# Kernel tuning notes

Hardware: AMD Instinct MI355X
Metric: run time of the kernel (lower is better)

## Reference

```python
import jax, jax.numpy as jnp
import numpy as np

B = 2048

def _conv(x, w, b, stride):
    y = jax.lax.conv_general_dilated(x, w, (stride, stride), 'VALID',
                                     dimension_numbers=('NCHW', 'OIHW', 'NCHW'))
    return y + b[None, :, None, None]

def _local_conv(x, w, b):
    # w: (Ho, Wo, Co, Ci, kh, kw), b: (Ho, Wo, Co); stride 1, valid
    Ho, Wo, Co, Ci, kh, kw = w.shape
    # patches: (B, Ci, kh*kw, Ho, Wo) -- sliding windows, small fixed loop over kernel taps
    patches = jnp.stack([x[:, :, i:i + Ho, j:j + Wo]
                         for i in range(kh) for j in range(kw)], axis=2)
    wf = w.reshape(Ho, Wo, Co, Ci, kh * kw)
    y = jnp.einsum('bcphw,hwocp->bohw', patches, wf)
    return y + jnp.transpose(b, (2, 0, 1))[None]

def setup_inputs() -> dict:
    key = jax.random.key(0)
    ks = jax.random.split(key, 18)
    s = 0.05
    inp = {
        'x': jax.random.normal(ks[0], (B, 5, 60, 60), dtype=jnp.float32),
        'info': jax.random.normal(ks[1], (B, 8), dtype=jnp.float32),
        'w1': jax.random.normal(ks[2], (32, 5, 3, 3), dtype=jnp.float32) * s,
        'b1': jnp.zeros((32,), dtype=jnp.float32),
        'w2a': jax.random.normal(ks[3], (64, 32, 3, 3), dtype=jnp.float32) * s,
        'b2a': jnp.zeros((64,), dtype=jnp.float32),
        'w2b': jax.random.normal(ks[4], (64, 64, 3, 3), dtype=jnp.float32) * s,
        'b2b': jnp.zeros((64,), dtype=jnp.float32),
        'lw3': jax.random.normal(ks[5], (9, 9, 64, 64, 5, 5), dtype=jnp.float32) * s,
        'lb3': jnp.zeros((9, 9, 64), dtype=jnp.float32),
        'lw4': jax.random.normal(ks[6], (5, 5, 64, 64, 5, 5), dtype=jnp.float32) * s,
        'lb4': jnp.zeros((5, 5, 64), dtype=jnp.float32),
        'lw5': jax.random.normal(ks[7], (3, 3, 64, 64, 3, 3), dtype=jnp.float32) * s,
        'lb5': jnp.zeros((3, 3, 64), dtype=jnp.float32),
        'hw': jax.random.normal(ks[8], (2, 584), dtype=jnp.float32) * s,
        'hb': jnp.zeros((2,), dtype=jnp.float32),
    }
    return inp

def reference(x, info, w1, b1, w2a, b2a, w2b, b2b, lw3, lb3, lw4, lb4, lw5, lb5, hw, hb):
    h = jnp.tanh(_conv(x, w1, b1, 2))            # (B,32,29,29)
    h = jnp.tanh(_conv(h, w2a, b2a, 1))          # (B,64,27,27)
    h = jnp.tanh(_conv(h, w2b, b2b, 2))          # (B,64,13,13)
    h = jnp.tanh(_local_conv(h, lw3, lb3))       # (B,64,9,9)
    h = jnp.tanh(_local_conv(h, lw4, lb4))       # (B,64,5,5)
    h = jnp.tanh(_local_conv(h, lw5, lb5))       # (B,64,3,3)
    h = h.reshape(h.shape[0], -1)                # (B,576)
    h = jnp.concatenate([h, info], axis=1)       # (B,584)
    logits = h @ hw.T + hb                       # (B,2)
    return jax.nn.softmax(logits, axis=1)
```

## Files before the change

kernel.cpp:

```cpp
#include <hip/hip_runtime.h>
#include <stdint.h>

#define THREADS 256

typedef short bf16x8 __attribute__((ext_vector_type(8)));
typedef float f32x4 __attribute__((ext_vector_type(4)));
typedef unsigned uint2_ __attribute__((ext_vector_type(2)));
typedef unsigned short ushort4_ __attribute__((ext_vector_type(4)));

#define GPTR(x) ((const __attribute__((address_space(1))) void*)(x))
#define LPTR(x) ((__attribute__((address_space(3))) void*)(x))

__device__ __forceinline__ unsigned short f2bf(float v) {
  unsigned u = __builtin_bit_cast(unsigned, v);
  u = (u + 0x7fff + ((u >> 16) & 1)) >> 16;
  return (unsigned short)u;
}
__device__ __forceinline__ float bf2f(unsigned short h) {
  return __builtin_bit_cast(float, (unsigned)h << 16);
}
__device__ __forceinline__ float fast_tanh(float x) {
  return 1.f - 2.f / (__expf(2.f * x) + 1.f);
}

__global__ void pack_w1t(const float* __restrict__ w1, float* __restrict__ w1t) {
  int idx = blockIdx.x * THREADS + threadIdx.x;
  if (idx >= 45 * 32) return;
  int t = idx >> 5, co = idx & 31;
  w1t[t * 32 + co] = w1[co * 45 + t];
}

__global__ void __launch_bounds__(256) conv1_direct(
    const float* __restrict__ x, const float* __restrict__ w1t,
    const float* __restrict__ bias, unsigned short* __restrict__ out, int Bc,
    int bstart) {
  constexpr int CI = 5, CO = 32, IH = 60, IW = 60, OH = 29, OW = 29;
  constexpr int RB = 8, NRB = 4;

  __shared__ unsigned short xs[CI * 17 * 60];

  const int tid = threadIdx.x;
  const int b = blockIdx.x / NRB;
  const int qb = blockIdx.x % NRB;
  const int oh0 = qb * RB;
  const int rows = min(RB, OH - oh0);
  const int ih0 = oh0 * 2;
  const int ihn = rows * 2 + 1;

  const float* xp = x + (size_t)(bstart + b) * (CI * IH * IW);

  const int nf4 = CI * ihn * 15;
  for (int i = tid; i < nf4; i += 256) {
    int col = i % 15;
    int row = i / 15;
    int ci = row / ihn, r = row % ihn;
    float4 v = ((const float4*)xp)[(ci * IH + ih0 + r) * 15 + col];
    ushort4_ o;
    o[0] = f2bf(v.x);
    o[1] = f2bf(v.y);
    o[2] = f2bf(v.z);
    o[3] = f2bf(v.w);
    ((ushort4_*)xs)[row * 15 + col] = o;
  }
  __syncthreads();

  if (tid >= rows * OW) return;
  const int r = tid / OW, c = tid % OW;
  const int base = (r * 2) * 60 + c * 2;
  const int cstr = ihn * 60;

  float acc[32];
#pragma unroll
  for (int co = 0; co < 32; co++) acc[co] = bias[co];

#pragma unroll
  for (int ci = 0; ci < CI; ci++)
#pragma unroll
    for (int kh = 0; kh < 3; kh++)
#pragma unroll
      for (int kw = 0; kw < 3; kw++) {
        const float v = bf2f(xs[ci * cstr + base + kh * 60 + kw]);
        const float* wt = w1t + ((ci * 3 + kh) * 3 + kw) * 32;
#pragma unroll
        for (int co = 0; co < 32; co++) acc[co] = fmaf(v, wt[co], acc[co]);
      }

  const int p = (oh0 + r) * OW + c;
  unsigned short* op = out + ((size_t)p * Bc + b) * CO;
#pragma unroll
  for (int cq = 0; cq < 4; cq++) {
    bf16x8 o;
#pragma unroll
    for (int j = 0; j < 8; j++) o[j] = (short)f2bf(fast_tanh(acc[cq * 8 + j]));
    *(bf16x8*)(op + cq * 8) = o;
  }
}

template <int CI, int KS>
__global__ void __launch_bounds__(THREADS) pack_w(const float* __restrict__ w,
                                                  unsigned short* __restrict__ wp,
                                                  int npos) {
  constexpr int K = CI * KS * KS;
  constexpr int S = K / 32;
  int idx = blockIdx.x * THREADS + threadIdx.x;
  int total = npos * S * 2048;
  if (idx >= total) return;
  int e = idx & 7;
  int lane = (idx >> 3) & 63;
  int mt = (idx >> 9) & 3;
  int rest = idx >> 11;
  int s = rest % S, pos = rest / S;
  int co = mt * 16 + (lane & 15);
  int k = s * 32 + (lane >> 4) * 8 + e;
  int tap = k / CI, ci = k % CI;
  int kh = tap / KS, kw = tap % KS;
  float v = w[((((size_t)pos * 64 + co) * CI + ci) * KS + kh) * KS + kw];
  wp[idx] = f2bf(v);
}

template <int CI, int IH, int IW, int OH, int OW, int KS, int ST, bool LOCAL, int BT>
__global__ void __launch_bounds__(256) conv_mfma(
    const unsigned short* __restrict__ X, const unsigned short* __restrict__ Wp,
    const float* __restrict__ bias, unsigned short* __restrict__ Y, int Bc) {
  constexpr int S = CI * KS * KS / 32;
  constexpr int NPOS = OH * OW;
  constexpr int BW = BT / 64;
  constexpr int CW = 4 / BW;
  constexpr int MT = 4 / CW;

  __shared__ unsigned short aT[2][2048];

  const int tid = threadIdx.x;
  const int lane = tid & 63;
  const int wu = tid >> 6;
  const int n = lane & 15, g = lane >> 4;
  const int bw = wu % BW, cw = wu / BW;

  int wg = blockIdx.x;
  {
    const int nwg = gridDim.x;
    const int q = nwg >> 3, rr = nwg & 7;
    const int xcd = wg & 7, l = wg >> 3;
    wg = (xcd < rr ? xcd * (q + 1) : rr * (q + 1) + (xcd - rr) * q) + l;
  }
  const int pos = wg % NPOS;
  const int btile = wg / NPOS;
  const int oh = pos / OW, ow = pos % OW;
  const int b0 = btile * BT + bw * 64;

  const unsigned short* Wpp = Wp + (LOCAL ? (size_t)pos * (S * 2048) : 0);

  f32x4 acc[MT][4] = {};

  const int bA = b0 + n;

  __builtin_amdgcn_global_load_lds(GPTR(Wpp + tid * 8), LPTR(&aT[0][tid * 8]), 16, 0, 0);

  int buf = 0;
  for (int s = 0; s < S; s++) {
    __syncthreads();
    if (s + 1 < S)
      __builtin_amdgcn_global_load_lds(GPTR(Wpp + (s + 1) * 2048 + tid * 8),
                                       LPTR(&aT[buf ^ 1][tid * 8]), 16, 0, 0);

    const int tap = (s * 32) / CI;
    const int ci0 = (s * 32) % CI + g * 8;
    const int kh = tap / KS, kw = tap % KS;
    const int pin = (oh * ST + kh) * IW + (ow * ST + kw);
    const unsigned short* xb = X + ((size_t)pin * Bc + bA) * CI + ci0;

    bf16x8 bfr[4];
#pragma unroll
    for (int j = 0; j < 4; j++) bfr[j] = *(const bf16x8*)(xb + j * 16 * CI);

    bf16x8 af[MT];
#pragma unroll
    for (int mt = 0; mt < MT; mt++)
      af[mt] = *(const bf16x8*)(&aT[buf][((cw * MT + mt) * 64 + lane) * 8]);

#pragma unroll
    for (int mt = 0; mt < MT; mt++)
#pragma unroll
      for (int j = 0; j < 4; j++)
        acc[mt][j] =
            __builtin_amdgcn_mfma_f32_16x16x32_bf16(af[mt], bfr[j], acc[mt][j], 0, 0, 0);
    buf ^= 1;
  }

#pragma unroll
  for (int mt = 0; mt < MT; mt++) {
#pragma unroll
    for (int j = 0; j < 4; j++) {
      unsigned short o[4];
#pragma unroll
      for (int r = 0; r < 4; r++) {
        const int co = (cw * MT + mt) * 16 + g * 4 + r;
        const float bv = LOCAL ? bias[pos * 64 + co] : bias[co];
        o[r] = f2bf(fast_tanh(acc[mt][j][r] + bv));
      }
      const int b = b0 + j * 16 + n;
      uint2_ pk;
      pk[0] = (unsigned)o[0] | ((unsigned)o[1] << 16);
      pk[1] = (unsigned)o[2] | ((unsigned)o[3] << 16);
      *(uint2_*)(Y + ((size_t)pos * Bc + b) * 64 + (cw * MT + mt) * 16 + g * 4) = pk;
    }
  }
}

__global__ void head_k(const unsigned short* __restrict__ h5,
                       const float* __restrict__ info, const float* __restrict__ hw,
                       const float* __restrict__ hb, float* __restrict__ out, int Bc,
                       int bstart) {
  int b = blockIdx.x * THREADS + threadIdx.x;
  if (b >= Bc) return;
  float l0 = hb[0], l1 = hb[1];
  for (int pos = 0; pos < 9; pos++) {
#pragma unroll
    for (int cb = 0; cb < 8; cb++) {
      bf16x8 v8 = *(const bf16x8*)(h5 + ((size_t)pos * Bc + b) * 64 + cb * 8);
#pragma unroll
      for (int j = 0; j < 8; j++) {
        float v = bf2f((unsigned short)v8[j]);
        int f = (cb * 8 + j) * 9 + pos;
        l0 = fmaf(v, hw[f], l0);
        l1 = fmaf(v, hw[584 + f], l1);
      }
    }
  }
#pragma unroll
  for (int k = 0; k < 8; k++) {
    float v = info[(size_t)(bstart + b) * 8 + k];
    l0 = fmaf(v, hw[576 + k], l0);
    l1 = fmaf(v, hw[584 + 576 + k], l1);
  }
  float m = fmaxf(l0, l1);
  float e0 = __expf(l0 - m), e1 = __expf(l1 - m);
  float s = e0 + e1;
  out[(size_t)(bstart + b) * 2 + 0] = e0 / s;
  out[(size_t)(bstart + b) * 2 + 1] = e1 / s;
}


extern "C" void kernel_launch(void* const* d_in, const int* in_sizes, int n_in,
                              void* d_out, int out_size, void* d_ws, size_t ws_size,
                              hipStream_t stream) {
  const float* x = (const float*)d_in[0];
  const float* info = (const float*)d_in[1];
  const float* w1 = (const float*)d_in[2];
  const float* b1 = (const float*)d_in[3];
  const float* w2a = (const float*)d_in[4];
  const float* b2a = (const float*)d_in[5];
  const float* w2b = (const float*)d_in[6];
  const float* b2b = (const float*)d_in[7];
  const float* lw3 = (const float*)d_in[8];
  const float* lb3 = (const float*)d_in[9];
  const float* lw4 = (const float*)d_in[10];
  const float* lb4 = (const float*)d_in[11];
  const float* lw5 = (const float*)d_in[12];
  const float* lb5 = (const float*)d_in[13];
  const float* hw = (const float*)d_in[14];
  const float* hb = (const float*)d_in[15];
  float* out = (float*)d_out;

  const int B = in_sizes[0] / 18000;

  const size_t SZ2A = 9ull * 2048, SZ2B = 18ull * 2048, SZ3 = 81ull * 50 * 2048,
               SZ4 = 25ull * 50 * 2048, SZ5 = 9ull * 18 * 2048;
  unsigned short* wp2a = (unsigned short*)d_ws;
  unsigned short* wp2b = wp2a + SZ2A;
  unsigned short* wp3 = wp2b + SZ2B;
  unsigned short* wp4 = wp3 + SZ3;
  unsigned short* wp5 = wp4 + SZ4;
  size_t wp_bytes = (SZ2A + SZ2B + SZ3 + SZ4 + SZ5) * 2;
  wp_bytes = (wp_bytes + 255) & ~(size_t)255;
  float* w1t = (float*)((char*)d_ws + wp_bytes);
  size_t w1t_bytes = ((45 * 32 * 4) + 255) & ~(size_t)255;

  const size_t per_sample = 53824 + 93312;
  int Bc = B;
  while (Bc > 256 && wp_bytes + w1t_bytes + (size_t)Bc * per_sample + 4096 > ws_size)
    Bc >>= 1;

  unsigned short* bufA = (unsigned short*)((char*)d_ws + wp_bytes + w1t_bytes);
  unsigned short* bufB =
      (unsigned short*)((char*)d_ws + wp_bytes + w1t_bytes + (size_t)Bc * 53824);

  hipLaunchKernelGGL(pack_w1t, dim3(6), dim3(THREADS), 0, stream, w1, w1t);
  hipLaunchKernelGGL((pack_w<32, 3>), dim3((SZ2A + 255) / 256), dim3(THREADS), 0, stream,
                     w2a, wp2a, 1);
  hipLaunchKernelGGL((pack_w<64, 3>), dim3((SZ2B + 255) / 256), dim3(THREADS), 0, stream,
                     w2b, wp2b, 1);
  hipLaunchKernelGGL((pack_w<64, 5>), dim3((SZ3 + 255) / 256), dim3(THREADS), 0, stream,
                     lw3, wp3, 81);
  hipLaunchKernelGGL((pack_w<64, 5>), dim3((SZ4 + 255) / 256), dim3(THREADS), 0, stream,
                     lw4, wp4, 25);
  hipLaunchKernelGGL((pack_w<64, 3>), dim3((SZ5 + 255) / 256), dim3(THREADS), 0, stream,
                     lw5, wp5, 9);

  const int nchunks = B / Bc;
  for (int c = 0; c < nchunks; c++) {
    const int bstart = c * Bc;

    hipLaunchKernelGGL(conv1_direct, dim3(Bc * 4), dim3(256), 0, stream, x, w1t, b1,
                       bufA, Bc, bstart);
    hipLaunchKernelGGL((conv_mfma<32, 29, 29, 27, 27, 3, 1, false, 256>),
                       dim3(729 * (Bc / 256)), dim3(256), 0, stream, bufA, wp2a, b2a,
                       bufB, Bc);
    hipLaunchKernelGGL((conv_mfma<64, 27, 27, 13, 13, 3, 2, false, 256>),
                       dim3(169 * (Bc / 256)), dim3(256), 0, stream, bufB, wp2b, b2b,
                       bufA, Bc);
    hipLaunchKernelGGL((conv_mfma<64, 13, 13, 9, 9, 5, 1, true, 256>),
                       dim3(81 * (Bc / 256)), dim3(256), 0, stream, bufA, wp3, lb3, bufB,
                       Bc);
    hipLaunchKernelGGL((conv_mfma<64, 9, 9, 5, 5, 5, 1, true, 128>),
                       dim3(25 * (Bc / 128)), dim3(256), 0, stream, bufB, wp4, lb4, bufA,
                       Bc);
    hipLaunchKernelGGL((conv_mfma<64, 5, 5, 3, 3, 3, 1, true, 64>),
                       dim3(9 * (Bc / 64)), dim3(256), 0, stream, bufA, wp5, lb5, bufB,
                       Bc);
    hipLaunchKernelGGL(head_k, dim3((Bc + THREADS - 1) / THREADS), dim3(THREADS), 0,
                       stream, bufB, info, hw, hb, out, Bc, bstart);
  }
}
```

Baseline: 574.4 us.

## Split conv1 output channels across waves with two-row blocks and fp32 LDS

Conv1 now processes two output rows per block instead of eight. Each of the four waves computes 8 of the 32 output channels for up to 58 pixels, where before each thread computed all 32 channels. The input tile is kept in fp32 shared memory instead of being converted to bf16, which removes the conversion work and the extra rounding. Grid size grows from 4 to 15 blocks per image, giving more parallelism and lower register pressure per thread, in exchange for more redundant input loads and six idle lanes per wave.

Measured after the change: 567.0 us. About the same (-1.3%).

```diff
diff --git a/kernel.cpp b/kernel.cpp
--- a/kernel.cpp
+++ b/kernel.cpp
@@ -35,15 +35,15 @@
     const float* __restrict__ bias, unsigned short* __restrict__ out, int Bc,
     int bstart) {
   constexpr int CI = 5, CO = 32, IH = 60, IW = 60, OH = 29, OW = 29;
-  constexpr int RB = 8, NRB = 4;
-
-  __shared__ unsigned short xs[CI * 17 * 60];
+  constexpr int RPB = 2, NRB = 15;
+
+  __shared__ float xs[CI * 5 * 60];
 
   const int tid = threadIdx.x;
   const int b = blockIdx.x / NRB;
   const int qb = blockIdx.x % NRB;
-  const int oh0 = qb * RB;
-  const int rows = min(RB, OH - oh0);
+  const int oh0 = qb * RPB;
+  const int rows = min(RPB, OH - oh0);
   const int ih0 = oh0 * 2;
   const int ihn = rows * 2 + 1;
 
@@ -54,24 +54,20 @@
     int col = i % 15;
     int row = i / 15;
     int ci = row / ihn, r = row % ihn;
-    float4 v = ((const float4*)xp)[(ci * IH + ih0 + r) * 15 + col];
-    ushort4_ o;
-    o[0] = f2bf(v.x);
-    o[1] = f2bf(v.y);
-    o[2] = f2bf(v.z);
-    o[3] = f2bf(v.w);
-    ((ushort4_*)xs)[row * 15 + col] = o;
+    ((float4*)xs)[row * 15 + col] = ((const float4*)xp)[(ci * IH + ih0 + r) * 15 + col];
   }
   __syncthreads();
 
-  if (tid >= rows * OW) return;
-  const int r = tid / OW, c = tid % OW;
+  const int lane = tid & 63;
+  const int wu = __builtin_amdgcn_readfirstlane(tid >> 6);
+  if (lane >= rows * OW) return;
+  const int r = lane / OW, c = lane % OW;
   const int base = (r * 2) * 60 + c * 2;
   const int cstr = ihn * 60;
 
-  float acc[32];
-#pragma unroll
-  for (int co = 0; co < 32; co++) acc[co] = bias[co];
+  float acc[8];
+#pragma unroll
+  for (int j = 0; j < 8; j++) acc[j] = bias[wu * 8 + j];
 
 #pragma unroll
   for (int ci = 0; ci < CI; ci++)
@@ -79,21 +75,17 @@
     for (int kh = 0; kh < 3; kh++)
 #pragma unroll
       for (int kw = 0; kw < 3; kw++) {
-        const float v = bf2f(xs[ci * cstr + base + kh * 60 + kw]);
-        const float* wt = w1t + ((ci * 3 + kh) * 3 + kw) * 32;
-#pragma unroll
-        for (int co = 0; co < 32; co++) acc[co] = fmaf(v, wt[co], acc[co]);
+        const float v = xs[ci * cstr + base + kh * 60 + kw];
+        const float* wt = w1t + ((ci * 3 + kh) * 3 + kw) * 32 + wu * 8;
+#pragma unroll
+        for (int j = 0; j < 8; j++) acc[j] = fmaf(v, wt[j], acc[j]);
       }
 
   const int p = (oh0 + r) * OW + c;
-  unsigned short* op = out + ((size_t)p * Bc + b) * CO;
-#pragma unroll
-  for (int cq = 0; cq < 4; cq++) {
-    bf16x8 o;
-#pragma unroll
-    for (int j = 0; j < 8; j++) o[j] = (short)f2bf(fast_tanh(acc[cq * 8 + j]));
-    *(bf16x8*)(op + cq * 8) = o;
-  }
+  bf16x8 o;
+#pragma unroll
+  for (int j = 0; j < 8; j++) o[j] = (short)f2bf(fast_tanh(acc[j]));
+  *(bf16x8*)(out + ((size_t)p * Bc + b) * CO + wu * 8) = o;
 }
 
 template <int CI, int KS>
@@ -301,7 +293,7 @@
   for (int c = 0; c < nchunks; c++) {
     const int bstart = c * Bc;
 
-    hipLaunchKernelGGL(conv1_direct, dim3(Bc * 4), dim3(256), 0, stream, x, w1t, b1,
+    hipLaunchKernelGGL(conv1_direct, dim3(Bc * 15), dim3(256), 0, stream, x, w1t, b1,
                        bufA, Bc, bstart);
     hipLaunchKernelGGL((conv_mfma<32, 29, 29, 27, 27, 3, 1, false, 256>),
                        dim3(729 * (Bc / 256)), dim3(256), 0, stream, bufA, wp2a, b2a,
```
